# Kernel optimization log

Measured on AMD Instinct MI355X. Metric: run time of the kernel, lower is better.

## Reference

```python
import jax, jax.numpy as jnp
import numpy as np

N_NODES = 50000
N_EDGES = 800000
NUM_FEATURES = 128
HIDDEN = 256
NUM_CLASSES = 64


def setup_inputs() -> dict:
    key = jax.random.key(0)
    k_x, k_e, k_w1, k_w2 = jax.random.split(key, 4)
    x = jax.random.normal(k_x, (N_NODES, NUM_FEATURES), dtype=jnp.float32)
    edge_index = jax.random.randint(k_e, (2, N_EDGES), 0, N_NODES, dtype=jnp.int64)
    # Glorot-style init for GCNConv weights
    W1 = jax.random.normal(k_w1, (NUM_FEATURES, HIDDEN), dtype=jnp.float32) * (1.0 / np.sqrt(NUM_FEATURES))
    b1 = jnp.zeros((HIDDEN,), dtype=jnp.float32)
    W2 = jax.random.normal(k_w2, (HIDDEN, NUM_CLASSES), dtype=jnp.float32) * (1.0 / np.sqrt(HIDDEN))
    b2 = jnp.zeros((NUM_CLASSES,), dtype=jnp.float32)
    return {"x": x, "edge_index": edge_index, "W1": W1, "b1": b1, "W2": W2, "b2": b2}


def reference(x, edge_index, W1, b1, W2, b2):
    N = x.shape[0]
    # GCNConv default: add self-loops, symmetric degree normalization
    loops = jnp.arange(N, dtype=edge_index.dtype)
    row = jnp.concatenate([edge_index[0], loops])  # source nodes [E+N]
    col = jnp.concatenate([edge_index[1], loops])  # target nodes [E+N]
    deg = jax.ops.segment_sum(jnp.ones(col.shape, dtype=x.dtype), col, num_segments=N)
    dinv = jnp.where(deg > 0, jax.lax.rsqrt(jnp.maximum(deg, 1e-12)), 0.0)
    norm = dinv[row] * dinv[col]  # [E+N]

    def gcn_conv(h, W, b):
        h = h @ W                         # [N, out] linear transform first
        msg = h[row] * norm[:, None]      # gather + edge normalization [E+N, out]
        agg = jax.ops.segment_sum(msg, col, num_segments=N)  # scatter-add [N, out]
        return agg + b

    h = jax.nn.relu(gcn_conv(x, W1, b1))
    return gcn_conv(h, W2, b2)
```

## Files before the change

### kernel.cpp

```cpp
#include <hip/hip_runtime.h>

#define N_NODES 50000
#define N_EDGES 800000
#define F_IN 128
#define F_HID 256
#define F_OUT 64

#define SCAN_NB ((N_NODES + 255) / 256)

#define OFF_ROWPTR 0ull
#define OFF_CNT    (256ull << 10)
#define OFF_DINV   (768ull << 10)
#define OFF_BSUM   (984ull << 10)
#define OFF_EIDX   (1ull << 20)
#define OFF_ELOC   ((2ull << 20) + (640ull << 10))
#define OFF_XB     ((4ull << 20) + (256ull << 10))
#define OFF_T2B    ((17ull << 20) + (512ull << 10))
#define OFF_W1F    (25ull << 20)
#define OFF_W2F    ((25ull << 20) + (128ull << 10))


typedef __attribute__((ext_vector_type(8))) short bfrag;
typedef __attribute__((ext_vector_type(4))) float f4acc;

__device__ __forceinline__ unsigned f2bf(float f) {
    unsigned u = __float_as_uint(f);
    return (u + 0x7FFFu + ((u >> 16) & 1u)) >> 16;
}
__device__ __forceinline__ float bflo(unsigned u) { return __uint_as_float(u << 16); }
__device__ __forceinline__ float bfhi(unsigned u) { return __uint_as_float(u & 0xFFFF0000u); }
__device__ __forceinline__ bfrag as_bfrag(uint4 v) {
    union { uint4 u; bfrag b; } x; x.u = v; return x.b;
}

__global__ __launch_bounds__(256) void wprep_zero_kernel(const float* __restrict__ W1,
                                                         const float* __restrict__ W2,
                                                         unsigned* __restrict__ W1f,
                                                         unsigned* __restrict__ W2f,
                                                         int* __restrict__ cnt) {
    int i = blockIdx.x * 256 + threadIdx.x;
    if (i < 16384) {
        int jj = i & 3, l = (i >> 2) & 63, nt = (i >> 8) & 15, ks = i >> 12;
        int k = ks * 32 + ((l >> 4) & 3) * 8 + 2 * jj;
        int n = nt * 16 + (l & 15);
        W1f[i] = f2bf(W1[(size_t)k * F_HID + n]) | (f2bf(W1[(size_t)(k + 1) * F_HID + n]) << 16);
    } else if (i < 24576) {
        int i2 = i - 16384;
        int jj = i2 & 3, l = (i2 >> 2) & 63, nt = (i2 >> 8) & 3, ks = i2 >> 10;
        int k = ks * 32 + ((l >> 4) & 3) * 8 + 2 * jj;
        int n = nt * 16 + (l & 15);
        W2f[i2] = f2bf(W2[(size_t)k * F_OUT + n]) | (f2bf(W2[(size_t)(k + 1) * F_OUT + n]) << 16);
    }
    if (i < N_NODES) cnt[i] = 0;
}


__global__ void hist_elocal_kernel(const int* __restrict__ cols, int* __restrict__ cnt,
                                   unsigned short* __restrict__ elocal, int e) {
    int i = blockIdx.x * blockDim.x + threadIdx.x;
    if (i < e) {
        int old = atomicAdd(&cnt[cols[i]], 1);
        elocal[i] = (unsigned short)old;
    }
}

__global__ __launch_bounds__(256) void bsum_kernel(const int* __restrict__ cnt, int* __restrict__ bsum) {
    __shared__ int s[256];
    int t = threadIdx.x;
    int i = blockIdx.x * 256 + t;
    int v = (i < N_NODES) ? cnt[i] : 0;
    s[t] = v;
    __syncthreads();
#pragma unroll
    for (int off = 128; off > 0; off >>= 1) {
        if (t < off) s[t] += s[t + off];
        __syncthreads();
    }
    if (t == 0) bsum[blockIdx.x] = s[0];
}

__global__ __launch_bounds__(256) void bscan_kernel(int* __restrict__ bsum) {
    __shared__ int s[256];
    int t = threadIdx.x;
    int v = (t < SCAN_NB) ? bsum[t] : 0;
    s[t] = v;
    __syncthreads();
#pragma unroll
    for (int off = 1; off < 256; off <<= 1) {
        int u = (t >= off) ? s[t - off] : 0;
        __syncthreads();
        s[t] += u;
        __syncthreads();
    }
    if (t < SCAN_NB) bsum[t] = s[t] - v;
}

__global__ __launch_bounds__(256) void rowptr_kernel(const int* __restrict__ cnt,
                                                     const int* __restrict__ bsum,
                                                     int* __restrict__ row_ptr,
                                                     float* __restrict__ dinv) {
    __shared__ int s[256];
    int t = threadIdx.x;
    int i = blockIdx.x * 256 + t;
    int v = (i < N_NODES) ? cnt[i] : 0;
    s[t] = v;
    __syncthreads();
#pragma unroll
    for (int off = 1; off < 256; off <<= 1) {
        int u = (t >= off) ? s[t - off] : 0;
        __syncthreads();
        s[t] += u;
        __syncthreads();
    }
    int excl = s[t] - v + bsum[blockIdx.x];
    if (i < N_NODES) {
        row_ptr[i] = excl;
        dinv[i] = rsqrtf((float)v + 1.0f);
    }
    if (blockIdx.x == 0 && t == 0) row_ptr[N_NODES] = N_EDGES;
}

__global__ void scatter_cvt_kernel(const int* __restrict__ rows, const int* __restrict__ cols,
                                   const int* __restrict__ row_ptr,
                                   const unsigned short* __restrict__ elocal,
                                   unsigned short* __restrict__ eidx,
                                   const float* __restrict__ x, const float* __restrict__ dinv,
                                   unsigned* __restrict__ xb) {
    int i = blockIdx.x * blockDim.x + threadIdx.x;
    if (i < N_EDGES) {
        int c = cols[i];
        int pos = row_ptr[c] + (int)elocal[i];
        eidx[pos] = (unsigned short)rows[i];
    }
    if (i < N_NODES * (F_IN / 8)) {
        int node = i >> 4;
        float d = dinv[node];
        float4 a = ((const float4*)x)[(size_t)i * 2];
        float4 b = ((const float4*)x)[(size_t)i * 2 + 1];
        uint4 o;
        o.x = f2bf(d * a.x) | (f2bf(d * a.y) << 16);
        o.y = f2bf(d * a.z) | (f2bf(d * a.w) << 16);
        o.z = f2bf(d * b.x) | (f2bf(d * b.y) << 16);
        o.w = f2bf(d * b.z) | (f2bf(d * b.w) << 16);
        ((uint4*)xb)[i] = o;
    }
}

__global__ __launch_bounds__(256, 4) void fused12_kernel(const unsigned* __restrict__ xb,
                                                         const int* __restrict__ row_ptr,
                                                         const unsigned short* __restrict__ eidx,
                                                         const float* __restrict__ dinv,
                                                         const uint4* __restrict__ W1f,
                                                         const float* __restrict__ b1,
                                                         const uint4* __restrict__ W2f,
                                                         unsigned short* __restrict__ t2b) {
    __shared__ __align__(16) char smem_raw[16896];
    unsigned* AxP = (unsigned*)smem_raw;
    unsigned short* HcS = (unsigned short*)smem_raw;

    int tid = threadIdx.x;
    int bm0 = blockIdx.x * 32;
    const uint4* xb4 = (const uint4*)xb;

    {
        int f8 = tid & 15;
        int ng = tid >> 4;
        for (int p = 0; p < 2; ++p) {
            int nl = p * 16 + ng;
            int c = bm0 + nl;
            float acc[8] = {};
            if (c < N_NODES) {
                uint4 S = xb4[(size_t)c * 16 + f8];
                acc[0] = bflo(S.x); acc[1] = bfhi(S.x);
                acc[2] = bflo(S.y); acc[3] = bfhi(S.y);
                acc[4] = bflo(S.z); acc[5] = bfhi(S.z);
                acc[6] = bflo(S.w); acc[7] = bfhi(S.w);
                int k = row_ptr[c];
                int k1 = row_ptr[c + 1];
                int kmain = k + ((k1 - k) & ~7);
                for (; k < kmain; k += 8) {
                    int r[8];
#pragma unroll
                    for (int j = 0; j < 8; ++j) r[j] = eidx[k + j];
                    uint4 U[8];
#pragma unroll
                    for (int j = 0; j < 8; ++j) U[j] = xb4[(size_t)r[j] * 16 + f8];
#pragma unroll
                    for (int j = 0; j < 8; ++j) {
                        acc[0] += bflo(U[j].x); acc[1] += bfhi(U[j].x);
                        acc[2] += bflo(U[j].y); acc[3] += bfhi(U[j].y);
                        acc[4] += bflo(U[j].z); acc[5] += bfhi(U[j].z);
                        acc[6] += bflo(U[j].w); acc[7] += bfhi(U[j].w);
                    }
                }
                if (k < k1) {
                    int r[8];
                    float m[8];
#pragma unroll
                    for (int j = 0; j < 8; ++j) {
                        int idx = (k + j < k1) ? k + j : k1 - 1;
                        r[j] = eidx[idx];
                        m[j] = (k + j < k1) ? 1.f : 0.f;
                    }
                    uint4 U[8];
#pragma unroll
                    for (int j = 0; j < 8; ++j) U[j] = xb4[(size_t)r[j] * 16 + f8];
#pragma unroll
                    for (int j = 0; j < 8; ++j) {
                        acc[0] = fmaf(m[j], bflo(U[j].x), acc[0]);
                        acc[1] = fmaf(m[j], bfhi(U[j].x), acc[1]);
                        acc[2] = fmaf(m[j], bflo(U[j].y), acc[2]);
                        acc[3] = fmaf(m[j], bfhi(U[j].y), acc[3]);
                        acc[4] = fmaf(m[j], bflo(U[j].z), acc[4]);
                        acc[5] = fmaf(m[j], bfhi(U[j].z), acc[5]);
                        acc[6] = fmaf(m[j], bflo(U[j].w), acc[6]);
                        acc[7] = fmaf(m[j], bfhi(U[j].w), acc[7]);
                    }
                }
                float dc = dinv[c];
#pragma unroll
                for (int q = 0; q < 8; ++q) acc[q] *= dc;
            }
            uint4 P;
            P.x = f2bf(acc[0]) | (f2bf(acc[1]) << 16);
            P.y = f2bf(acc[2]) | (f2bf(acc[3]) << 16);
            P.z = f2bf(acc[4]) | (f2bf(acc[5]) << 16);
            P.w = f2bf(acc[6]) | (f2bf(acc[7]) << 16);
            *(uint4*)&AxP[nl * 68 + f8 * 4] = P;
        }
    }
    __syncthreads();

    int w = tid >> 6;
    int l = tid & 63;
    int mtile = w >> 1;
    int nhalf = w & 1;
    int lr = l & 15;
    int lq = l >> 4;

    f4acc acc1[8] = {};
#pragma unroll
    for (int ks = 0; ks < 4; ++ks) {
        bfrag a = as_bfrag(*(const uint4*)&AxP[(mtile * 16 + lr) * 68 + ks * 16 + lq * 4]);
#pragma unroll
        for (int nt = 0; nt < 8; ++nt) {
            bfrag b = as_bfrag(W1f[(ks * 16 + nhalf * 8 + nt) * 64 + l]);
            acc1[nt] = __builtin_amdgcn_mfma_f32_16x16x32_bf16(a, b, acc1[nt], 0, 0, 0);
        }
    }
    __syncthreads();

#pragma unroll
    for (int nt = 0; nt < 8; ++nt) {
        int col = nhalf * 128 + nt * 16 + lr;
        float bias = b1[col];
#pragma unroll
        for (int r = 0; r < 4; ++r) {
            int row = mtile * 16 + lq * 4 + r;
            float v = fmaxf(acc1[nt][r] + bias, 0.f);
            HcS[row * 264 + col] = (unsigned short)f2bf(v);
        }
    }
    __syncthreads();

    f4acc acc2[2] = {};
#pragma unroll
    for (int ks = 0; ks < 8; ++ks) {
        bfrag a = as_bfrag(*(const uint4*)&HcS[(mtile * 16 + lr) * 264 + ks * 32 + lq * 8]);
#pragma unroll
        for (int nt = 0; nt < 2; ++nt) {
            bfrag b = as_bfrag(W2f[(ks * 4 + nhalf * 2 + nt) * 64 + l]);
            acc2[nt] = __builtin_amdgcn_mfma_f32_16x16x32_bf16(a, b, acc2[nt], 0, 0, 0);
        }
    }

#pragma unroll
    for (int nt = 0; nt < 2; ++nt) {
        int col = nhalf * 32 + nt * 16 + lr;
#pragma unroll
        for (int r = 0; r < 4; ++r) {
            int row = bm0 + mtile * 16 + lq * 4 + r;
            if (row < N_NODES) {
                float d = dinv[row];
                t2b[(size_t)row * 64 + col] = (unsigned short)f2bf(d * acc2[nt][r]);
            }
        }
    }
}

__global__ __launch_bounds__(256) void l2_gather_kernel(const unsigned* __restrict__ t2b,
                                                        const int* __restrict__ row_ptr,
                                                        const unsigned short* __restrict__ eidx,
                                                        const float* __restrict__ dinv,
                                                        const float* __restrict__ b2,
                                                        float* __restrict__ out) {
    int tid = threadIdx.x;
    int f8 = tid & 7;
    int nl = tid >> 3;
    int c = blockIdx.x * 32 + nl;
    if (c >= N_NODES) return;
    uint4 S = ((const uint4*)t2b)[(size_t)c * 8 + f8];
    float acc[8];
    acc[0] = bflo(S.x); acc[1] = bfhi(S.x);
    acc[2] = bflo(S.y); acc[3] = bfhi(S.y);
    acc[4] = bflo(S.z); acc[5] = bfhi(S.z);
    acc[6] = bflo(S.w); acc[7] = bfhi(S.w);
    int k = row_ptr[c];
    int k1 = row_ptr[c + 1];
    int kmain = k + ((k1 - k) & ~15);
    for (; k < kmain; k += 16) {
        int r[16];
#pragma unroll
        for (int j = 0; j < 16; ++j) r[j] = eidx[k + j];
        uint4 U[16];
#pragma unroll
        for (int j = 0; j < 16; ++j) U[j] = ((const uint4*)t2b)[(size_t)r[j] * 8 + f8];
#pragma unroll
        for (int j = 0; j < 16; ++j) {
            acc[0] += bflo(U[j].x); acc[1] += bfhi(U[j].x);
            acc[2] += bflo(U[j].y); acc[3] += bfhi(U[j].y);
            acc[4] += bflo(U[j].z); acc[5] += bfhi(U[j].z);
            acc[6] += bflo(U[j].w); acc[7] += bfhi(U[j].w);
        }
    }
    for (; k < k1; k += 8) {
        int r[8];
        float m[8];
#pragma unroll
        for (int j = 0; j < 8; ++j) {
            int idx = (k + j < k1) ? k + j : k1 - 1;
            r[j] = eidx[idx];
            m[j] = (k + j < k1) ? 1.f : 0.f;
        }
        uint4 U[8];
#pragma unroll
        for (int j = 0; j < 8; ++j) U[j] = ((const uint4*)t2b)[(size_t)r[j] * 8 + f8];
#pragma unroll
        for (int j = 0; j < 8; ++j) {
            acc[0] = fmaf(m[j], bflo(U[j].x), acc[0]);
            acc[1] = fmaf(m[j], bfhi(U[j].x), acc[1]);
            acc[2] = fmaf(m[j], bflo(U[j].y), acc[2]);
            acc[3] = fmaf(m[j], bfhi(U[j].y), acc[3]);
            acc[4] = fmaf(m[j], bflo(U[j].z), acc[4]);
            acc[5] = fmaf(m[j], bfhi(U[j].z), acc[5]);
            acc[6] = fmaf(m[j], bflo(U[j].w), acc[6]);
            acc[7] = fmaf(m[j], bfhi(U[j].w), acc[7]);
        }
    }
    float dc = dinv[c];
    float4 b2a = *(const float4*)&b2[f8 * 8];
    float4 b2b = *(const float4*)&b2[f8 * 8 + 4];
    float4 o0, o1;
    o0.x = fmaf(dc, acc[0], b2a.x);
    o0.y = fmaf(dc, acc[1], b2a.y);
    o0.z = fmaf(dc, acc[2], b2a.z);
    o0.w = fmaf(dc, acc[3], b2a.w);
    o1.x = fmaf(dc, acc[4], b2b.x);
    o1.y = fmaf(dc, acc[5], b2b.y);
    o1.z = fmaf(dc, acc[6], b2b.z);
    o1.w = fmaf(dc, acc[7], b2b.w);
    ((float4*)out)[(size_t)c * 16 + f8 * 2] = o0;
    ((float4*)out)[(size_t)c * 16 + f8 * 2 + 1] = o1;
}


extern "C" void kernel_launch(void* const* d_in, const int* in_sizes, int n_in,
                              void* d_out, int out_size, void* d_ws, size_t ws_size,
                              hipStream_t stream) {
    const float* x = (const float*)d_in[0];
    const int* edge_index = (const int*)d_in[1];
    const float* W1 = (const float*)d_in[2];
    const float* b1 = (const float*)d_in[3];
    const float* W2 = (const float*)d_in[4];
    const float* b2 = (const float*)d_in[5];
    float* out = (float*)d_out;

    const int* rows = edge_index;
    const int* cols = edge_index + N_EDGES;

    char* ws = (char*)d_ws;
    int* row_ptr = (int*)(ws + OFF_ROWPTR);
    int* cnt = (int*)(ws + OFF_CNT);
    float* dinv = (float*)(ws + OFF_DINV);
    int* bsum = (int*)(ws + OFF_BSUM);
    unsigned short* eidx = (unsigned short*)(ws + OFF_EIDX);
    unsigned short* elocal = (unsigned short*)(ws + OFF_ELOC);
    unsigned* xb = (unsigned*)(ws + OFF_XB);
    unsigned* t2b = (unsigned*)(ws + OFF_T2B);
    unsigned* W1f = (unsigned*)(ws + OFF_W1F);
    unsigned* W2f = (unsigned*)(ws + OFF_W2F);

    const int BT = 256;

    wprep_zero_kernel<<<SCAN_NB, 256, 0, stream>>>(W1, W2, W1f, W2f, cnt);
    hist_elocal_kernel<<<(N_EDGES + BT - 1) / BT, BT, 0, stream>>>(cols, cnt, elocal, N_EDGES);
    bsum_kernel<<<SCAN_NB, 256, 0, stream>>>(cnt, bsum);
    bscan_kernel<<<1, 256, 0, stream>>>(bsum);
    rowptr_kernel<<<SCAN_NB, 256, 0, stream>>>(cnt, bsum, row_ptr, dinv);
    scatter_cvt_kernel<<<(N_EDGES + BT - 1) / BT, BT, 0, stream>>>(
        rows, cols, row_ptr, elocal, eidx, x, dinv, xb);

    fused12_kernel<<<(N_NODES + 31) / 32, 256, 0, stream>>>(
        xb, row_ptr, eidx, dinv, (const uint4*)W1f, b1, (const uint4*)W2f, (unsigned short*)t2b);
    l2_gather_kernel<<<(N_NODES + 31) / 32, 256, 0, stream>>>(t2b, row_ptr, eidx, dinv, b2, out);
}
```

Measured before the change: 123.6 us.

## Split fused layer-1 gather+GEMM into separate gather and GEMM kernels

```diff
diff --git a/kernel.cpp b/kernel.cpp
--- a/kernel.cpp
+++ b/kernel.cpp
@@ -18,6 +18,7 @@
 #define OFF_T2B    ((17ull << 20) + (512ull << 10))
 #define OFF_W1F    (25ull << 20)
 #define OFF_W2F    ((25ull << 20) + (128ull << 10))
+#define OFF_AXG    (26ull << 20)
 
 
 typedef __attribute__((ext_vector_type(8))) short bfrag;
@@ -146,90 +147,86 @@
     }
 }
 
-__global__ __launch_bounds__(256, 4) void fused12_kernel(const unsigned* __restrict__ xb,
-                                                         const int* __restrict__ row_ptr,
-                                                         const unsigned short* __restrict__ eidx,
-                                                         const float* __restrict__ dinv,
-                                                         const uint4* __restrict__ W1f,
-                                                         const float* __restrict__ b1,
-                                                         const uint4* __restrict__ W2f,
-                                                         unsigned short* __restrict__ t2b) {
-    __shared__ __align__(16) char smem_raw[16896];
-    unsigned* AxP = (unsigned*)smem_raw;
-    unsigned short* HcS = (unsigned short*)smem_raw;
+__global__ __launch_bounds__(256) void gather_kernel(const unsigned* __restrict__ xb,
+                                                     const int* __restrict__ row_ptr,
+                                                     const unsigned short* __restrict__ eidx,
+                                                     const float* __restrict__ dinv,
+                                                     unsigned* __restrict__ AxG) {
+    int gid = blockIdx.x * 256 + threadIdx.x;
+    if (gid >= N_NODES * 16) return;
+    int c = gid >> 4;
+    int f8 = gid & 15;
+    const uint4* xb4 = (const uint4*)xb;
+
+    float acc[8];
+    uint4 S = xb4[(size_t)c * 16 + f8];
+    acc[0] = bflo(S.x); acc[1] = bfhi(S.x);
+    acc[2] = bflo(S.y); acc[3] = bfhi(S.y);
+    acc[4] = bflo(S.z); acc[5] = bfhi(S.z);
+    acc[6] = bflo(S.w); acc[7] = bfhi(S.w);
+    int k = row_ptr[c];
+    int k1 = row_ptr[c + 1];
+    int kmain = k + ((k1 - k) & ~7);
+    for (; k < kmain; k += 8) {
+        int r[8];
+#pragma unroll
+        for (int j = 0; j < 8; ++j) r[j] = eidx[k + j];
+        uint4 U[8];
+#pragma unroll
+        for (int j = 0; j < 8; ++j) U[j] = xb4[(size_t)r[j] * 16 + f8];
+#pragma unroll
+        for (int j = 0; j < 8; ++j) {
+            acc[0] += bflo(U[j].x); acc[1] += bfhi(U[j].x);
+            acc[2] += bflo(U[j].y); acc[3] += bfhi(U[j].y);
+            acc[4] += bflo(U[j].z); acc[5] += bfhi(U[j].z);
+            acc[6] += bflo(U[j].w); acc[7] += bfhi(U[j].w);
+        }
+    }
+    if (k < k1) {
+        int r[8];
+        float m[8];
+#pragma unroll
+        for (int j = 0; j < 8; ++j) {
+            int idx = (k + j < k1) ? k + j : k1 - 1;
+            r[j] = eidx[idx];
+            m[j] = (k + j < k1) ? 1.f : 0.f;
+        }
+        uint4 U[8];
+#pragma unroll
+        for (int j = 0; j < 8; ++j) U[j] = xb4[(size_t)r[j] * 16 + f8];
+#pragma unroll
+        for (int j = 0; j < 8; ++j) {
+            acc[0] = fmaf(m[j], bflo(U[j].x), acc[0]);
+            acc[1] = fmaf(m[j], bfhi(U[j].x), acc[1]);
+            acc[2] = fmaf(m[j], bflo(U[j].y), acc[2]);
+            acc[3] = fmaf(m[j], bfhi(U[j].y), acc[3]);
+            acc[4] = fmaf(m[j], bflo(U[j].z), acc[4]);
+            acc[5] = fmaf(m[j], bfhi(U[j].z), acc[5]);
+            acc[6] = fmaf(m[j], bflo(U[j].w), acc[6]);
+            acc[7] = fmaf(m[j], bfhi(U[j].w), acc[7]);
+        }
+    }
+    float dc = dinv[c];
+#pragma unroll
+    for (int q = 0; q < 8; ++q) acc[q] *= dc;
+    uint4 P;
+    P.x = f2bf(acc[0]) | (f2bf(acc[1]) << 16);
+    P.y = f2bf(acc[2]) | (f2bf(acc[3]) << 16);
+    P.z = f2bf(acc[4]) | (f2bf(acc[5]) << 16);
+    P.w = f2bf(acc[6]) | (f2bf(acc[7]) << 16);
+    ((uint4*)AxG)[(size_t)c * 16 + f8] = P;
+}
+
+__global__ __launch_bounds__(256, 4) void gemm12_kernel(const uint4* __restrict__ AxG,
+                                                        const uint4* __restrict__ W1f,
+                                                        const float* __restrict__ b1,
+                                                        const uint4* __restrict__ W2f,
+                                                        const float* __restrict__ dinv,
+                                                        unsigned short* __restrict__ t2b) {
+    __shared__ unsigned short HcS[32 * 264];
 
     int tid = threadIdx.x;
     int bm0 = blockIdx.x * 32;
-    const uint4* xb4 = (const uint4*)xb;
-
-    {
-        int f8 = tid & 15;
-        int ng = tid >> 4;
-        for (int p = 0; p < 2; ++p) {
-            int nl = p * 16 + ng;
-            int c = bm0 + nl;
-            float acc[8] = {};
-            if (c < N_NODES) {
-                uint4 S = xb4[(size_t)c * 16 + f8];
-                acc[0] = bflo(S.x); acc[1] = bfhi(S.x);
-                acc[2] = bflo(S.y); acc[3] = bfhi(S.y);
-                acc[4] = bflo(S.z); acc[5] = bfhi(S.z);
-                acc[6] = bflo(S.w); acc[7] = bfhi(S.w);
-                int k = row_ptr[c];
-                int k1 = row_ptr[c + 1];
-                int kmain = k + ((k1 - k) & ~7);
-                for (; k < kmain; k += 8) {
-                    int r[8];
-#pragma unroll
-                    for (int j = 0; j < 8; ++j) r[j] = eidx[k + j];
-                    uint4 U[8];
-#pragma unroll
-                    for (int j = 0; j < 8; ++j) U[j] = xb4[(size_t)r[j] * 16 + f8];
-#pragma unroll
-                    for (int j = 0; j < 8; ++j) {
-                        acc[0] += bflo(U[j].x); acc[1] += bfhi(U[j].x);
-                        acc[2] += bflo(U[j].y); acc[3] += bfhi(U[j].y);
-                        acc[4] += bflo(U[j].z); acc[5] += bfhi(U[j].z);
-                        acc[6] += bflo(U[j].w); acc[7] += bfhi(U[j].w);
-                    }
-                }
-                if (k < k1) {
-                    int r[8];
-                    float m[8];
-#pragma unroll
-                    for (int j = 0; j < 8; ++j) {
-                        int idx = (k + j < k1) ? k + j : k1 - 1;
-                        r[j] = eidx[idx];
-                        m[j] = (k + j < k1) ? 1.f : 0.f;
-                    }
-                    uint4 U[8];
-#pragma unroll
-                    for (int j = 0; j < 8; ++j) U[j] = xb4[(size_t)r[j] * 16 + f8];
-#pragma unroll
-                    for (int j = 0; j < 8; ++j) {
-                        acc[0] = fmaf(m[j], bflo(U[j].x), acc[0]);
-                        acc[1] = fmaf(m[j], bfhi(U[j].x), acc[1]);
-                        acc[2] = fmaf(m[j], bflo(U[j].y), acc[2]);
-                        acc[3] = fmaf(m[j], bfhi(U[j].y), acc[3]);
-                        acc[4] = fmaf(m[j], bflo(U[j].z), acc[4]);
-                        acc[5] = fmaf(m[j], bfhi(U[j].z), acc[5]);
-                        acc[6] = fmaf(m[j], bflo(U[j].w), acc[6]);
-                        acc[7] = fmaf(m[j], bfhi(U[j].w), acc[7]);
-                    }
-                }
-                float dc = dinv[c];
-#pragma unroll
-                for (int q = 0; q < 8; ++q) acc[q] *= dc;
-            }
-            uint4 P;
-            P.x = f2bf(acc[0]) | (f2bf(acc[1]) << 16);
-            P.y = f2bf(acc[2]) | (f2bf(acc[3]) << 16);
-            P.z = f2bf(acc[4]) | (f2bf(acc[5]) << 16);
-            P.w = f2bf(acc[6]) | (f2bf(acc[7]) << 16);
-            *(uint4*)&AxP[nl * 68 + f8 * 4] = P;
-        }
-    }
-    __syncthreads();
 
     int w = tid >> 6;
     int l = tid & 63;
@@ -238,17 +235,19 @@
     int lr = l & 15;
     int lq = l >> 4;
 
+    int arow = bm0 + mtile * 16 + lr;
+    if (arow >= N_NODES) arow = 0;
+
     f4acc acc1[8] = {};
 #pragma unroll
     for (int ks = 0; ks < 4; ++ks) {
-        bfrag a = as_bfrag(*(const uint4*)&AxP[(mtile * 16 + lr) * 68 + ks * 16 + lq * 4]);
+        bfrag a = as_bfrag(AxG[(size_t)arow * 16 + ks * 4 + lq]);
 #pragma unroll
         for (int nt = 0; nt < 8; ++nt) {
             bfrag b = as_bfrag(W1f[(ks * 16 + nhalf * 8 + nt) * 64 + l]);
             acc1[nt] = __builtin_amdgcn_mfma_f32_16x16x32_bf16(a, b, acc1[nt], 0, 0, 0);
         }
     }
-    __syncthreads();
 
 #pragma unroll
     for (int nt = 0; nt < 8; ++nt) {
@@ -389,6 +388,7 @@
     unsigned* t2b = (unsigned*)(ws + OFF_T2B);
     unsigned* W1f = (unsigned*)(ws + OFF_W1F);
     unsigned* W2f = (unsigned*)(ws + OFF_W2F);
+    unsigned* AxG = (unsigned*)(ws + OFF_AXG);
 
     const int BT = 256;
 
@@ -400,7 +400,8 @@
     scatter_cvt_kernel<<<(N_EDGES + BT - 1) / BT, BT, 0, stream>>>(
         rows, cols, row_ptr, elocal, eidx, x, dinv, xb);
 
-    fused12_kernel<<<(N_NODES + 31) / 32, 256, 0, stream>>>(
-        xb, row_ptr, eidx, dinv, (const uint4*)W1f, b1, (const uint4*)W2f, (unsigned short*)t2b);
+    gather_kernel<<<(N_NODES * 16 + BT - 1) / BT, BT, 0, stream>>>(xb, row_ptr, eidx, dinv, AxG);
+    gemm12_kernel<<<(N_NODES + 31) / 32, 256, 0, stream>>>(
+        (const uint4*)AxG, (const uint4*)W1f, b1, (const uint4*)W2f, dinv, (unsigned short*)t2b);
     l2_gather_kernel<<<(N_NODES + 31) / 32, 256, 0, stream>>>(t2b, row_ptr, eidx, dinv, b2, out);
 }
```

Result: slower. 128.8 us (+4.2%).
